# Kernel tuning notes

Measured on AMD Instinct MI355X. Metric: run time of the kernel, lower is better.

## Reference

```python
import jax, jax.numpy as jnp
import numpy as np

N, IN_DIM, HID, LAT, E = 8192, 512, 256, 128, 262144


def gcn_conv(x, W, b, src, dst, n):
    # PyG-style GCNConv: linear transform, add self-loops, D^-1/2 A D^-1/2 aggregation, bias.
    h = x @ W                                                  # [n, out]
    loops = jnp.arange(n)
    s = jnp.concatenate([src, loops])
    d = jnp.concatenate([dst, loops])
    deg = jax.ops.segment_sum(jnp.ones(s.shape[0], x.dtype), d, num_segments=n)
    dinv = jnp.where(deg > 0, jax.lax.rsqrt(deg), jnp.zeros((), x.dtype))
    norm = dinv[s] * dinv[d]                                   # [E+n]
    out = jax.ops.segment_sum(h[s] * norm[:, None], d, num_segments=n)
    return out + b


def setup_inputs() -> dict:
    key = jax.random.key(0)
    ks = jax.random.split(key, 9)
    x = jax.random.normal(ks[0], (N, IN_DIM), dtype=jnp.float32)
    edge_index = jax.random.randint(ks[1], (2, E), 0, N, dtype=jnp.int64)
    eps = jax.random.normal(ks[2], (N, LAT), dtype=jnp.float32)
    # Glorot-ish scaled params
    W1 = jax.random.normal(ks[3], (IN_DIM, HID), dtype=jnp.float32) / np.sqrt(IN_DIM)
    b1 = jnp.zeros((HID,), jnp.float32)
    Wmu = jax.random.normal(ks[4], (HID, LAT), dtype=jnp.float32) / np.sqrt(HID)
    bmu = jnp.zeros((LAT,), jnp.float32)
    Wls = jax.random.normal(ks[5], (HID, LAT), dtype=jnp.float32) / np.sqrt(HID)
    bls = jnp.zeros((LAT,), jnp.float32)
    return {"x": x, "edge_index": edge_index, "eps": eps,
            "W1": W1, "b1": b1, "Wmu": Wmu, "bmu": bmu, "Wls": Wls, "bls": bls}


def reference(x, edge_index, eps, W1, b1, Wmu, bmu, Wls, bls):
    src, dst = edge_index[0], edge_index[1]
    n = x.shape[0]
    h = jax.nn.relu(gcn_conv(x, W1, b1, src, dst, n))          # [N, HID]
    mu = gcn_conv(h, Wmu, bmu, src, dst, n)                    # [N, LAT]
    logstd = gcn_conv(h, Wls, bls, src, dst, n)                # [N, LAT]
    z = eps * jnp.exp(logstd) + mu                             # reparametrize (training mode)
    adj_recon = jax.nn.sigmoid(z @ z.T)                        # [N, N]
    return adj_recon, mu, logstd
```

## Files before the change

### kernel.cpp

```cpp
#include <hip/hip_runtime.h>

#define N_NODES 8192
#define IN_DIM  512
#define HID     256
#define LAT     128
#define NEDGE   262144

typedef __attribute__((ext_vector_type(8))) short  bf16x8;
typedef __attribute__((ext_vector_type(4))) float  f32x4;
typedef unsigned short u16;
typedef __attribute__((ext_vector_type(4))) unsigned short u16x4;

static __device__ inline u16 f2bf(float f) {
    unsigned u = __float_as_uint(f);
    unsigned r = (u + 0x7fffu + ((u >> 16) & 1u)) >> 16;
    return (u16)r;
}
static __device__ inline float bf2f(u16 s) {
    return __uint_as_float(((unsigned)s) << 16);
}


__global__ __launch_bounds__(256) void count_kernel(const int* __restrict__ dst,
                                                    int* __restrict__ cnt) {
    int e = blockIdx.x * 256 + threadIdx.x;
    atomicAdd(&cnt[dst[e]], 1);
}

__global__ __launch_bounds__(256) void dinv_kernel(const int* __restrict__ cnt,
                                                   float* __restrict__ dinv) {
    int v = blockIdx.x * 256 + threadIdx.x;
    dinv[v] = rsqrtf((float)cnt[v] + 1.0f);
}

__global__ __launch_bounds__(256) void scan_kernel(const int* __restrict__ cnt,
                                                   int* __restrict__ rowptr,
                                                   int* __restrict__ cursor) {
    __shared__ int part[256];
    const int t = threadIdx.x;
    const int base = t * 32;
    int local[32];
    int s = 0;
#pragma unroll
    for (int i = 0; i < 32; ++i) { local[i] = s; s += cnt[base + i]; }
    part[t] = s;
    __syncthreads();
    for (int off = 1; off < 256; off <<= 1) {
        int v = 0;
        if (t >= off) v = part[t - off];
        __syncthreads();
        if (t >= off) part[t] += v;
        __syncthreads();
    }
    int pre = (t == 0) ? 0 : part[t - 1];
#pragma unroll
    for (int i = 0; i < 32; ++i) {
        int r = pre + local[i];
        rowptr[base + i] = r;
        cursor[base + i] = r;
    }
    if (t == 255) rowptr[8192] = part[255];
}

__global__ __launch_bounds__(256) void fill_kernel(const int* __restrict__ src,
                                                   const int* __restrict__ dst,
                                                   int* __restrict__ cursor,
                                                   int* __restrict__ ebuf) {
    int e = blockIdx.x * 256 + threadIdx.x;
    int pos = atomicAdd(&cursor[dst[e]], 1);
    ebuf[pos] = src[e];
}


__global__ __launch_bounds__(256) void convx_kernel(const float* __restrict__ X,
                                                    u16* __restrict__ xh,
                                                    u16* __restrict__ xl) {
    int t = blockIdx.x * 256 + threadIdx.x;
    f32x4 v = *(const f32x4*)(X + (size_t)t * 4);
    u16x4 h, l;
#pragma unroll
    for (int j = 0; j < 4; ++j) {
        h[j] = f2bf(v[j]);
        l[j] = f2bf(v[j] - bf2f(h[j]));
    }
    *(u16x4*)(xh + (size_t)t * 4) = h;
    *(u16x4*)(xl + (size_t)t * 4) = l;
}

__global__ __launch_bounds__(256) void convw_kernel(const float* __restrict__ W,
                                                    u16* __restrict__ th,
                                                    u16* __restrict__ tl,
                                                    int K, int N, int Kld, int roff) {
    int e = blockIdx.x * 256 + threadIdx.x;
    if (e >= K * N) return;
    int k = e / N, n = e - k * N;
    float f = W[e];
    u16 hi = f2bf(f);
    u16 lo = f2bf(f - bf2f(hi));
    size_t o = (size_t)(roff + n) * Kld + k;
    th[o] = hi;
    tl[o] = lo;
}

__global__ __launch_bounds__(256) void gemm_mfma(const u16* __restrict__ Ah,
                                                 const u16* __restrict__ Al,
                                                 const u16* __restrict__ Bth,
                                                 const u16* __restrict__ Btl,
                                                 float* __restrict__ C,
                                                 int K, int ldc) {
    const int lane = threadIdx.x & 63;
    const int wave = threadIdx.x >> 6;
    const int l16 = lane & 15, quad = lane >> 4;
    const int rowBase = blockIdx.y * 128 + (wave >> 1) * 64;
    const int colBase = blockIdx.x * 128 + (wave & 1) * 64;

    f32x4 acc[4][4] = {};

    for (int k0 = 0; k0 < K; k0 += 32) {
        const int kk = k0 + quad * 8;
        bf16x8 ah[4], al[4], bh[4], bl[4];
#pragma unroll
        for (int r = 0; r < 4; ++r) {
            int row = rowBase + r * 16 + l16;
            ah[r] = *(const bf16x8*)(Ah + (size_t)row * K + kk);
            al[r] = *(const bf16x8*)(Al + (size_t)row * K + kk);
        }
#pragma unroll
        for (int c = 0; c < 4; ++c) {
            int row = colBase + c * 16 + l16;
            bh[c] = *(const bf16x8*)(Bth + (size_t)row * K + kk);
            bl[c] = *(const bf16x8*)(Btl + (size_t)row * K + kk);
        }
#pragma unroll
        for (int r = 0; r < 4; ++r)
#pragma unroll
            for (int c = 0; c < 4; ++c) {
                acc[r][c] = __builtin_amdgcn_mfma_f32_16x16x32_bf16(ah[r], bh[c], acc[r][c], 0, 0, 0);
                acc[r][c] = __builtin_amdgcn_mfma_f32_16x16x32_bf16(ah[r], bl[c], acc[r][c], 0, 0, 0);
                acc[r][c] = __builtin_amdgcn_mfma_f32_16x16x32_bf16(al[r], bh[c], acc[r][c], 0, 0, 0);
            }
    }

#pragma unroll
    for (int r = 0; r < 4; ++r)
#pragma unroll
        for (int c = 0; c < 4; ++c)
#pragma unroll
            for (int i = 0; i < 4; ++i) {
                int orow = rowBase + r * 16 + quad * 4 + i;
                int ocol = colBase + c * 16 + l16;
                C[(size_t)orow * ldc + ocol] = acc[r][c][i];
            }
}

__global__ __launch_bounds__(256) void gather1_kernel(const float* __restrict__ pre1,
                                                      u16* __restrict__ h1h,
                                                      u16* __restrict__ h1l,
                                                      const int* __restrict__ rowptr,
                                                      const int* __restrict__ ebuf,
                                                      const float* __restrict__ dinv,
                                                      const float* __restrict__ b1) {
    const int wave = threadIdx.x >> 6, lane = threadIdx.x & 63;
    const int v = blockIdx.x * 4 + wave;
    const int c = lane * 4;
    const float dv = dinv[v];
    f32x4 acc = *(const f32x4*)(pre1 + (size_t)v * HID + c);
    acc *= dv * dv;
    int i = rowptr[v], end = rowptr[v + 1];
    for (; i + 1 < end; i += 2) {
        int s0 = ebuf[i], s1 = ebuf[i + 1];
        float n0 = dv * dinv[s0], n1 = dv * dinv[s1];
        f32x4 h0 = *(const f32x4*)(pre1 + (size_t)s0 * HID + c);
        f32x4 h1v = *(const f32x4*)(pre1 + (size_t)s1 * HID + c);
#pragma unroll
        for (int j = 0; j < 4; ++j) acc[j] += n0 * h0[j] + n1 * h1v[j];
    }
    if (i < end) {
        int s0 = ebuf[i];
        float n0 = dv * dinv[s0];
        f32x4 h0 = *(const f32x4*)(pre1 + (size_t)s0 * HID + c);
#pragma unroll
        for (int j = 0; j < 4; ++j) acc[j] += n0 * h0[j];
    }
    f32x4 bb = *(const f32x4*)(b1 + c);
    u16x4 hv, lv;
#pragma unroll
    for (int j = 0; j < 4; ++j) {
        float h = fmaxf(acc[j] + bb[j], 0.0f);
        hv[j] = f2bf(h);
        lv[j] = f2bf(h - bf2f(hv[j]));
    }
    *(u16x4*)(h1h + (size_t)v * HID + c) = hv;
    *(u16x4*)(h1l + (size_t)v * HID + c) = lv;
}

__global__ __launch_bounds__(256) void gather2_kernel(const float* __restrict__ pre2,
                                                      const int* __restrict__ rowptr,
                                                      const int* __restrict__ ebuf,
                                                      const float* __restrict__ dinv,
                                                      const float* __restrict__ bmu,
                                                      const float* __restrict__ bls,
                                                      const float* __restrict__ eps,
                                                      float* __restrict__ out_mu,
                                                      float* __restrict__ out_ls,
                                                      u16* __restrict__ zhi,
                                                      u16* __restrict__ zlo) {
    const int wave = threadIdx.x >> 6, lane = threadIdx.x & 63;
    const int v = blockIdx.x * 4 + wave;
    const int c = lane * 4;
    const float dv = dinv[v];
    f32x4 acc = *(const f32x4*)(pre2 + (size_t)v * HID + c);
    acc *= dv * dv;
    int i = rowptr[v], end = rowptr[v + 1];
    for (; i + 1 < end; i += 2) {
        int s0 = ebuf[i], s1 = ebuf[i + 1];
        float n0 = dv * dinv[s0], n1 = dv * dinv[s1];
        f32x4 h0 = *(const f32x4*)(pre2 + (size_t)s0 * HID + c);
        f32x4 h1v = *(const f32x4*)(pre2 + (size_t)s1 * HID + c);
#pragma unroll
        for (int j = 0; j < 4; ++j) acc[j] += n0 * h0[j] + n1 * h1v[j];
    }
    if (i < end) {
        int s0 = ebuf[i];
        float n0 = dv * dinv[s0];
        f32x4 h0 = *(const f32x4*)(pre2 + (size_t)s0 * HID + c);
#pragma unroll
        for (int j = 0; j < 4; ++j) acc[j] += n0 * h0[j];
    }
    const float* bias = (lane < 32) ? (bmu + c) : (bls + (c - 128));
    f32x4 bb = *(const f32x4*)bias;
#pragma unroll
    for (int j = 0; j < 4; ++j) acc[j] += bb[j];

    f32x4 other;
#pragma unroll
    for (int j = 0; j < 4; ++j) other[j] = __shfl(acc[j], (lane + 32) & 63, 64);

    if (lane < 32) {
        int idx = v * LAT + c;
        f32x4 ep = *(const f32x4*)(eps + idx);
        __builtin_nontemporal_store(acc, (f32x4*)(out_mu + idx));
        u16x4 hv, lv;
#pragma unroll
        for (int j = 0; j < 4; ++j) {
            float z = ep[j] * __expf(other[j]) + acc[j];
            u16 hi = f2bf(z);
            hv[j] = hi;
            lv[j] = f2bf(z - bf2f(hi));
        }
        *(u16x4*)(zhi + idx) = hv;
        *(u16x4*)(zlo + idx) = lv;
    } else {
        int idx = v * LAT + (c - 128);
        __builtin_nontemporal_store(acc, (f32x4*)(out_ls + idx));
    }
}

#define NTRI 2080
__global__ __launch_bounds__(256) void zzt_kernel(const u16* __restrict__ zhi,
                                                  const u16* __restrict__ zlo,
                                                  float* __restrict__ out) {
    const int lane = threadIdx.x & 63;
    const int wave = threadIdx.x >> 6;
    const int l16 = lane & 15, quad = lane >> 4;

    int bid = (blockIdx.x & 7) * 260 + (blockIdx.x >> 3);
    int by = (int)((sqrtf(8.0f * (float)bid + 1.0f) - 1.0f) * 0.5f);
    while ((by + 1) * (by + 2) / 2 <= bid) ++by;
    while (by * (by + 1) / 2 > bid) --by;
    const int bx = bid - by * (by + 1) / 2;

    const int rowBase = by * 128 + (wave >> 1) * 64;
    const int colBase = bx * 128 + (wave & 1) * 64;

    f32x4 acc[4][4] = {};

#pragma unroll
    for (int k0 = 0; k0 < LAT; k0 += 32) {
        const int kk = k0 + quad * 8;
        bf16x8 ah[4], al[4], bh[4], bl[4];
#pragma unroll
        for (int r = 0; r < 4; ++r) {
            int row = rowBase + r * 16 + l16;
            ah[r] = *(const bf16x8*)(zhi + (size_t)row * LAT + kk);
            al[r] = *(const bf16x8*)(zlo + (size_t)row * LAT + kk);
        }
#pragma unroll
        for (int c = 0; c < 4; ++c) {
            int row = colBase + c * 16 + l16;
            bh[c] = *(const bf16x8*)(zhi + (size_t)row * LAT + kk);
            bl[c] = *(const bf16x8*)(zlo + (size_t)row * LAT + kk);
        }
#pragma unroll
        for (int r = 0; r < 4; ++r)
#pragma unroll
            for (int c = 0; c < 4; ++c) {
                acc[r][c] = __builtin_amdgcn_mfma_f32_16x16x32_bf16(ah[r], bh[c], acc[r][c], 0, 0, 0);
                acc[r][c] = __builtin_amdgcn_mfma_f32_16x16x32_bf16(ah[r], bl[c], acc[r][c], 0, 0, 0);
                acc[r][c] = __builtin_amdgcn_mfma_f32_16x16x32_bf16(al[r], bh[c], acc[r][c], 0, 0, 0);
            }
    }

    const bool offdiag = (by != bx);
#pragma unroll
    for (int r = 0; r < 4; ++r)
#pragma unroll
        for (int c = 0; c < 4; ++c) {
            f32x4 sig;
#pragma unroll
            for (int i = 0; i < 4; ++i)
                sig[i] = 1.0f / (1.0f + __expf(-acc[r][c][i]));
#pragma unroll
            for (int i = 0; i < 4; ++i) {
                int orow = rowBase + r * 16 + quad * 4 + i;
                int ocol = colBase + c * 16 + l16;
                __builtin_nontemporal_store(sig[i], out + (size_t)orow * N_NODES + ocol);
            }
            if (offdiag) {
                int trow = colBase + c * 16 + l16;
                int tcol = rowBase + r * 16 + quad * 4;
                __builtin_nontemporal_store(sig, (f32x4*)(out + (size_t)trow * N_NODES + tcol));
            }
        }
}

extern "C" void kernel_launch(void* const* d_in, const int* in_sizes, int n_in,
                              void* d_out, int out_size, void* d_ws, size_t ws_size,
                              hipStream_t stream) {
    const float* x   = (const float*)d_in[0];
    const int*   ei  = (const int*)d_in[1];
    const float* eps = (const float*)d_in[2];
    const float* W1  = (const float*)d_in[3];
    const float* b1  = (const float*)d_in[4];
    const float* Wmu = (const float*)d_in[5];
    const float* bmu = (const float*)d_in[6];
    const float* Wls = (const float*)d_in[7];
    const float* bls = (const float*)d_in[8];
    const int* src = ei;
    const int* dst = ei + NEDGE;

    float* out = (float*)d_out;
    float* pre1 = out;
    float* pre2 = out + 2097152;
    int*   ibase  = (int*)(out + 4194304);
    int*   cnt    = ibase;
    int*   rowptr = ibase + 8192;
    int*   cursor = ibase + 16385;
    int*   ebuf   = ibase + 24577;
    u16* xhi    = (u16*)(out + 4587520);
    u16* xlo    = (u16*)(out + 6684672);
    u16* h1hi   = (u16*)(out + 8781824);
    u16* h1lo   = (u16*)(out + 9830400);
    u16* w1thi  = (u16*)(out + 10878976);
    u16* w1tlo  = (u16*)(out + 11010048);
    u16* wcathi = (u16*)(out + 11141120);
    u16* wcatlo = (u16*)(out + 11173888);
    float* out_mu = out + 67108864;
    float* out_ls = out + 68157440;

    float* dinv = (float*)d_ws;
    u16* zhi = (u16*)((char*)d_ws + 32768);
    u16* zlo = (u16*)((char*)d_ws + 32768 + 2097152);

    hipMemsetAsync(cnt, 0, 8192 * sizeof(int), stream);

    count_kernel<<<NEDGE / 256, 256, 0, stream>>>(dst, cnt);
    dinv_kernel<<<N_NODES / 256, 256, 0, stream>>>(cnt, dinv);
    scan_kernel<<<1, 256, 0, stream>>>(cnt, rowptr, cursor);
    fill_kernel<<<NEDGE / 256, 256, 0, stream>>>(src, dst, cursor, ebuf);

    convx_kernel<<<4096, 256, 0, stream>>>(x, xhi, xlo);
    convw_kernel<<<(IN_DIM * HID) / 256, 256, 0, stream>>>(W1, w1thi, w1tlo, IN_DIM, HID, IN_DIM, 0);
    convw_kernel<<<(HID * LAT) / 256, 256, 0, stream>>>(Wmu, wcathi, wcatlo, HID, LAT, HID, 0);
    convw_kernel<<<(HID * LAT) / 256, 256, 0, stream>>>(Wls, wcathi, wcatlo, HID, LAT, HID, LAT);

    gemm_mfma<<<dim3(HID / 128, N_NODES / 128), 256, 0, stream>>>(xhi, xlo, w1thi, w1tlo,
                                                                  pre1, IN_DIM, HID);
    gather1_kernel<<<N_NODES / 4, 256, 0, stream>>>(pre1, h1hi, h1lo, rowptr, ebuf, dinv, b1);

    gemm_mfma<<<dim3(HID / 128, N_NODES / 128), 256, 0, stream>>>(h1hi, h1lo, wcathi, wcatlo,
                                                                  pre2, HID, HID);

    gather2_kernel<<<N_NODES / 4, 256, 0, stream>>>(pre2, rowptr, ebuf, dinv, bmu, bls, eps,
                                                    out_mu, out_ls, zhi, zlo);

    zzt_kernel<<<NTRI, 256, 0, stream>>>(zhi, zlo, out);
}
```

Measured before the change: 526.2 us.

## Merge prep kernels, co-schedule edge fill with GEMM1, and coalesce zzt stores via LDS

```diff
diff --git a/kernel.cpp b/kernel.cpp
--- a/kernel.cpp
+++ b/kernel.cpp
@@ -20,29 +20,73 @@
     return __uint_as_float(((unsigned)s) << 16);
 }
 
-
-__global__ __launch_bounds__(256) void count_kernel(const int* __restrict__ dst,
-                                                    int* __restrict__ cnt) {
-    int e = blockIdx.x * 256 + threadIdx.x;
-    atomicAdd(&cnt[dst[e]], 1);
-}
-
-__global__ __launch_bounds__(256) void dinv_kernel(const int* __restrict__ cnt,
-                                                   float* __restrict__ dinv) {
-    int v = blockIdx.x * 256 + threadIdx.x;
-    dinv[v] = rsqrtf((float)cnt[v] + 1.0f);
+#define PREP_BLOCKS 5888
+
+static __device__ inline void convw_body(const float* __restrict__ W,
+                                         u16* __restrict__ th,
+                                         u16* __restrict__ tl,
+                                         int K, int N, int Kld, int roff, int e) {
+    if (e >= K * N) return;
+    int k = e / N, n = e - k * N;
+    float f = W[e];
+    u16 hi = f2bf(f);
+    u16 lo = f2bf(f - bf2f(hi));
+    size_t o = (size_t)(roff + n) * Kld + k;
+    th[o] = hi;
+    tl[o] = lo;
+}
+
+__global__ __launch_bounds__(256) void prep_kernel(const int* __restrict__ dst,
+                                                   int* __restrict__ cnt,
+                                                   const float* __restrict__ X,
+                                                   u16* __restrict__ xh,
+                                                   u16* __restrict__ xl,
+                                                   const float* __restrict__ W1,
+                                                   u16* __restrict__ w1h,
+                                                   u16* __restrict__ w1l,
+                                                   const float* __restrict__ Wmu,
+                                                   const float* __restrict__ Wls,
+                                                   u16* __restrict__ wch,
+                                                   u16* __restrict__ wcl) {
+    const int b = blockIdx.x, t = threadIdx.x;
+    if (b < 1024) {
+        int e = b * 256 + t;
+        atomicAdd(&cnt[dst[e]], 1);
+    } else if (b < 5120) {
+        int idx = (b - 1024) * 256 + t;
+        f32x4 v = *(const f32x4*)(X + (size_t)idx * 4);
+        u16x4 h, l;
+#pragma unroll
+        for (int j = 0; j < 4; ++j) {
+            h[j] = f2bf(v[j]);
+            l[j] = f2bf(v[j] - bf2f(h[j]));
+        }
+        *(u16x4*)(xh + (size_t)idx * 4) = h;
+        *(u16x4*)(xl + (size_t)idx * 4) = l;
+    } else if (b < 5632) {
+        convw_body(W1, w1h, w1l, IN_DIM, HID, IN_DIM, 0, (b - 5120) * 256 + t);
+    } else if (b < 5760) {
+        convw_body(Wmu, wch, wcl, HID, LAT, HID, 0, (b - 5632) * 256 + t);
+    } else {
+        convw_body(Wls, wch, wcl, HID, LAT, HID, LAT, (b - 5760) * 256 + t);
+    }
 }
 
 __global__ __launch_bounds__(256) void scan_kernel(const int* __restrict__ cnt,
                                                    int* __restrict__ rowptr,
-                                                   int* __restrict__ cursor) {
+                                                   int* __restrict__ cursor,
+                                                   float* __restrict__ dinv) {
     __shared__ int part[256];
     const int t = threadIdx.x;
     const int base = t * 32;
     int local[32];
     int s = 0;
 #pragma unroll
-    for (int i = 0; i < 32; ++i) { local[i] = s; s += cnt[base + i]; }
+    for (int i = 0; i < 32; ++i) {
+        int cv = cnt[base + i];
+        local[i] = s; s += cv;
+        dinv[base + i] = rsqrtf((float)cv + 1.0f);
+    }
     part[t] = s;
     __syncthreads();
     for (int off = 1; off < 256; off <<= 1) {
@@ -62,57 +106,17 @@
     if (t == 255) rowptr[8192] = part[255];
 }
 
-__global__ __launch_bounds__(256) void fill_kernel(const int* __restrict__ src,
-                                                   const int* __restrict__ dst,
-                                                   int* __restrict__ cursor,
-                                                   int* __restrict__ ebuf) {
-    int e = blockIdx.x * 256 + threadIdx.x;
-    int pos = atomicAdd(&cursor[dst[e]], 1);
-    ebuf[pos] = src[e];
-}
-
-
-__global__ __launch_bounds__(256) void convx_kernel(const float* __restrict__ X,
-                                                    u16* __restrict__ xh,
-                                                    u16* __restrict__ xl) {
-    int t = blockIdx.x * 256 + threadIdx.x;
-    f32x4 v = *(const f32x4*)(X + (size_t)t * 4);
-    u16x4 h, l;
-#pragma unroll
-    for (int j = 0; j < 4; ++j) {
-        h[j] = f2bf(v[j]);
-        l[j] = f2bf(v[j] - bf2f(h[j]));
-    }
-    *(u16x4*)(xh + (size_t)t * 4) = h;
-    *(u16x4*)(xl + (size_t)t * 4) = l;
-}
-
-__global__ __launch_bounds__(256) void convw_kernel(const float* __restrict__ W,
-                                                    u16* __restrict__ th,
-                                                    u16* __restrict__ tl,
-                                                    int K, int N, int Kld, int roff) {
-    int e = blockIdx.x * 256 + threadIdx.x;
-    if (e >= K * N) return;
-    int k = e / N, n = e - k * N;
-    float f = W[e];
-    u16 hi = f2bf(f);
-    u16 lo = f2bf(f - bf2f(hi));
-    size_t o = (size_t)(roff + n) * Kld + k;
-    th[o] = hi;
-    tl[o] = lo;
-}
-
-__global__ __launch_bounds__(256) void gemm_mfma(const u16* __restrict__ Ah,
-                                                 const u16* __restrict__ Al,
-                                                 const u16* __restrict__ Bth,
-                                                 const u16* __restrict__ Btl,
-                                                 float* __restrict__ C,
-                                                 int K, int ldc) {
-    const int lane = threadIdx.x & 63;
-    const int wave = threadIdx.x >> 6;
+static __device__ inline void gemm_body(const u16* __restrict__ Ah,
+                                        const u16* __restrict__ Al,
+                                        const u16* __restrict__ Bth,
+                                        const u16* __restrict__ Btl,
+                                        float* __restrict__ C,
+                                        int K, int ldc, int bx, int by, int tid) {
+    const int lane = tid & 63;
+    const int wave = tid >> 6;
     const int l16 = lane & 15, quad = lane >> 4;
-    const int rowBase = blockIdx.y * 128 + (wave >> 1) * 64;
-    const int colBase = blockIdx.x * 128 + (wave & 1) * 64;
+    const int rowBase = by * 128 + (wave >> 1) * 64;
+    const int colBase = bx * 128 + (wave & 1) * 64;
 
     f32x4 acc[4][4] = {};
 
@@ -151,6 +155,33 @@
                 int ocol = colBase + c * 16 + l16;
                 C[(size_t)orow * ldc + ocol] = acc[r][c][i];
             }
+}
+
+__global__ __launch_bounds__(256) void fillgemm_kernel(const u16* __restrict__ xh,
+                                                       const u16* __restrict__ xl,
+                                                       const u16* __restrict__ w1h,
+                                                       const u16* __restrict__ w1l,
+                                                       float* __restrict__ pre1,
+                                                       const int* __restrict__ src,
+                                                       const int* __restrict__ dst,
+                                                       int* __restrict__ cursor,
+                                                       int* __restrict__ ebuf) {
+    const int b = blockIdx.x;
+    if (b < 128) {
+        gemm_body(xh, xl, w1h, w1l, pre1, IN_DIM, HID, b & 1, b >> 1, threadIdx.x);
+    } else {
+        int e = (b - 128) * 256 + threadIdx.x;
+        int pos = atomicAdd(&cursor[dst[e]], 1);
+        ebuf[pos] = src[e];
+    }
+}
+
+__global__ __launch_bounds__(256) void gemm2_kernel(const u16* __restrict__ h1h,
+                                                    const u16* __restrict__ h1l,
+                                                    const u16* __restrict__ wch,
+                                                    const u16* __restrict__ wcl,
+                                                    float* __restrict__ pre2) {
+    gemm_body(h1h, h1l, wch, wcl, pre2, HID, HID, blockIdx.x & 1, blockIdx.x >> 1, threadIdx.x);
 }
 
 __global__ __launch_bounds__(256) void gather1_kernel(const float* __restrict__ pre1,
@@ -260,6 +291,7 @@
 __global__ __launch_bounds__(256) void zzt_kernel(const u16* __restrict__ zhi,
                                                   const u16* __restrict__ zlo,
                                                   float* __restrict__ out) {
+    __shared__ float lds[4][16][68];
     const int lane = threadIdx.x & 63;
     const int wave = threadIdx.x >> 6;
     const int l16 = lane & 15, quad = lane >> 4;
@@ -301,27 +333,45 @@
             }
     }
 
-    const bool offdiag = (by != bx);
 #pragma unroll
     for (int r = 0; r < 4; ++r)
 #pragma unroll
+        for (int c = 0; c < 4; ++c)
+#pragma unroll
+            for (int i = 0; i < 4; ++i)
+                acc[r][c][i] = 1.0f / (1.0f + __expf(-acc[r][c][i]));
+
+#pragma unroll
+    for (int r = 0; r < 4; ++r) {
+#pragma unroll
+        for (int c = 0; c < 4; ++c)
+#pragma unroll
+            for (int i = 0; i < 4; ++i)
+                lds[wave][quad * 4 + i][c * 16 + l16] = acc[r][c][i];
+#pragma unroll
+        for (int it = 0; it < 4; ++it) {
+            f32x4 v = *(const f32x4*)&lds[wave][it * 4 + quad][l16 * 4];
+            int orow = rowBase + r * 16 + it * 4 + quad;
+            __builtin_nontemporal_store(v, (f32x4*)(out + (size_t)orow * N_NODES + colBase + l16 * 4));
+        }
+    }
+
+    if (by != bx) {
+#pragma unroll
         for (int c = 0; c < 4; ++c) {
-            f32x4 sig;
-#pragma unroll
-            for (int i = 0; i < 4; ++i)
-                sig[i] = 1.0f / (1.0f + __expf(-acc[r][c][i]));
-#pragma unroll
-            for (int i = 0; i < 4; ++i) {
-                int orow = rowBase + r * 16 + quad * 4 + i;
-                int ocol = colBase + c * 16 + l16;
-                __builtin_nontemporal_store(sig[i], out + (size_t)orow * N_NODES + ocol);
+#pragma unroll
+            for (int r = 0; r < 4; ++r) {
+                f32x4 tv = acc[r][c];
+                *(f32x4*)&lds[wave][l16][r * 16 + quad * 4] = tv;
             }
-            if (offdiag) {
-                int trow = colBase + c * 16 + l16;
-                int tcol = rowBase + r * 16 + quad * 4;
-                __builtin_nontemporal_store(sig, (f32x4*)(out + (size_t)trow * N_NODES + tcol));
+#pragma unroll
+            for (int it = 0; it < 4; ++it) {
+                f32x4 v = *(const f32x4*)&lds[wave][it * 4 + quad][l16 * 4];
+                int orow = colBase + c * 16 + it * 4 + quad;
+                __builtin_nontemporal_store(v, (f32x4*)(out + (size_t)orow * N_NODES + rowBase + l16 * 4));
             }
         }
+    }
 }
 
 extern "C" void kernel_launch(void* const* d_in, const int* in_sizes, int n_in,
@@ -364,22 +414,17 @@
 
     hipMemsetAsync(cnt, 0, 8192 * sizeof(int), stream);
 
-    count_kernel<<<NEDGE / 256, 256, 0, stream>>>(dst, cnt);
-    dinv_kernel<<<N_NODES / 256, 256, 0, stream>>>(cnt, dinv);
-    scan_kernel<<<1, 256, 0, stream>>>(cnt, rowptr, cursor);
-    fill_kernel<<<NEDGE / 256, 256, 0, stream>>>(src, dst, cursor, ebuf);
-
-    convx_kernel<<<4096, 256, 0, stream>>>(x, xhi, xlo);
-    convw_kernel<<<(IN_DIM * HID) / 256, 256, 0, stream>>>(W1, w1thi, w1tlo, IN_DIM, HID, IN_DIM, 0);
-    convw_kernel<<<(HID * LAT) / 256, 256, 0, stream>>>(Wmu, wcathi, wcatlo, HID, LAT, HID, 0);
-    convw_kernel<<<(HID * LAT) / 256, 256, 0, stream>>>(Wls, wcathi, wcatlo, HID, LAT, HID, LAT);
-
-    gemm_mfma<<<dim3(HID / 128, N_NODES / 128), 256, 0, stream>>>(xhi, xlo, w1thi, w1tlo,
-                                                                  pre1, IN_DIM, HID);
+    prep_kernel<<<PREP_BLOCKS, 256, 0, stream>>>(dst, cnt, x, xhi, xlo,
+                                                 W1, w1thi, w1tlo, Wmu, Wls, wcathi, wcatlo);
+
+    scan_kernel<<<1, 256, 0, stream>>>(cnt, rowptr, cursor, dinv);
+
+    fillgemm_kernel<<<128 + 1024, 256, 0, stream>>>(xhi, xlo, w1thi, w1tlo, pre1,
+                                                    src, dst, cursor, ebuf);
+
     gather1_kernel<<<N_NODES / 4, 256, 0, stream>>>(pre1, h1hi, h1lo, rowptr, ebuf, dinv, b1);
 
-    gemm_mfma<<<dim3(HID / 128, N_NODES / 128), 256, 0, stream>>>(h1hi, h1lo, wcathi, wcatlo,
-                                                                  pre2, HID, HID);
+    gemm2_kernel<<<128, 256, 0, stream>>>(h1hi, h1lo, wcathi, wcatlo, pre2);
 
     gather2_kernel<<<N_NODES / 4, 256, 0, stream>>>(pre2, rowptr, ebuf, dinv, bmu, bls, eps,
                                                     out_mu, out_ls, zhi, zlo);
```

Measured after the change: 495.5 us. 5.8% less time.
